# Kernel tuning notes

Hardware: AMD Instinct MI355X
Metric: run time of the kernel (lower is better)

## Reference

```python
import jax, jax.numpy as jnp
import numpy as np

N_EXPERTS = 64
LN_EPS = 1e-5


def _layer_norm(x, gamma, beta, eps=LN_EPS):
    mu = jnp.mean(x, axis=-1, keepdims=True)
    var = jnp.mean(jnp.square(x - mu), axis=-1, keepdims=True)
    return (x - mu) * jax.lax.rsqrt(var + eps) * gamma + beta


def setup_inputs() -> dict:
    key = jax.random.key(0)
    ks = jax.random.split(key, 4)
    B, T, D, Ff = 2, 1024, 512, 2048
    x = jax.random.normal(ks[0], (B, T, D), dtype=jnp.float32)
    hex_weights = jax.random.uniform(ks[1], (B, T, N_EXPERTS), dtype=jnp.float32)
    W_in = jax.random.normal(ks[2], (N_EXPERTS, Ff, D), dtype=jnp.float32) * (D ** -0.5)
    b_in = jnp.zeros((N_EXPERTS, Ff), dtype=jnp.float32)
    W_out = jax.random.normal(ks[3], (N_EXPERTS, D, Ff), dtype=jnp.float32) * (Ff ** -0.5)
    b_out = jnp.zeros((N_EXPERTS, D), dtype=jnp.float32)
    ln_gamma = jnp.ones((D,), dtype=jnp.float32)
    ln_beta = jnp.zeros((D,), dtype=jnp.float32)
    return {"x": x, "hex_weights": hex_weights, "W_in": W_in, "b_in": b_in,
            "W_out": W_out, "b_out": b_out, "ln_gamma": ln_gamma,
            "ln_beta": ln_beta, "top_k": 4}


def reference(x, hex_weights, W_in, b_in, W_out, b_out, ln_gamma, ln_beta, top_k):
    B, T, D = x.shape
    N = B * T
    x_n = _layer_norm(x, ln_gamma, ln_beta)

    # top-k routing; renormalize the selected weights (matches torch topk + sum-norm)
    top_w, top_idx = jax.lax.top_k(hex_weights, top_k)          # (B,T,k)
    top_w = top_w / (jnp.sum(top_w, axis=-1, keepdims=True) + 1e-8)

    x_flat = x_n.reshape(N, D)
    # Scatter the k normalized weights into a dense (N, 64) routing matrix.
    # Non-selected experts get weight 0, so a dense per-expert sweep computes
    # EXACTLY the same combined output as the per-token gather in the original.
    w_full = jnp.zeros((N, N_EXPERTS), dtype=x.dtype)
    w_full = w_full.at[jnp.arange(N)[:, None], top_idx.reshape(N, top_k)].set(
        top_w.reshape(N, top_k))

    def body(acc, e):
        W_in_e, b_in_e, W_out_e, b_out_e, we = e  # we: (N,)
        h = jax.nn.silu(x_flat @ W_in_e.T + b_in_e)            # (N, d_ff)
        acc = acc + we[:, None] * (h @ W_out_e.T + b_out_e)    # (N, D)
        return acc, None

    acc, _ = jax.lax.scan(body, jnp.zeros_like(x_flat),
                          (W_in, b_in, W_out, b_out, w_full.T))
    return acc.reshape(B, T, D)
```

## Files before the change

kernel.cpp:

```cpp
#include <hip/hip_runtime.h>

#define NTOK 2048
#define DD   512
#define FFD  2048
#define NE   64
#define KSEL 4
#define NPAIR (NTOK*KSEL)
#define BM 192
#define BN 128
#define BK 64
#define MAX_TILES 128
#define HROWS (NPAIR + 256)

typedef short s16x8 __attribute__((ext_vector_type(8)));
typedef float f32x4 __attribute__((ext_vector_type(4)));

typedef const __attribute__((address_space(1))) char* gptr_t;
typedef __attribute__((address_space(3))) char* lptr_t;

static __device__ __forceinline__ unsigned short f2bf(float f) {
    unsigned int u = __builtin_bit_cast(unsigned int, f);
    u += 0x7FFFu + ((u >> 16) & 1u);
    return (unsigned short)(u >> 16);
}

__global__ __launch_bounds__(256) void k_ln_route(
    const float* __restrict__ x, const float* __restrict__ hw,
    const float* __restrict__ gamma, const float* __restrict__ beta,
    unsigned short* __restrict__ xn_bf, int* __restrict__ counts,
    int* __restrict__ tok_e, float* __restrict__ tok_w)
{
    const int t = blockIdx.x;
    const int tid = threadIdx.x;
    const float* xr = x + (size_t)t * DD;
    float v0 = xr[tid];
    float v1 = xr[tid + 256];
    float s = v0 + v1, s2 = v0*v0 + v1*v1;
    #pragma unroll
    for (int off = 32; off > 0; off >>= 1) {
        s  += __shfl_down(s, off);
        s2 += __shfl_down(s2, off);
    }
    __shared__ float rsum[4], rsum2[4];
    __shared__ float smu, srs;
    const int wid = tid >> 6, lane = tid & 63;
    if (lane == 0) { rsum[wid] = s; rsum2[wid] = s2; }
    __syncthreads();
    if (tid == 0) {
        float a = 0.f, b = 0.f;
        for (int i = 0; i < 4; ++i) { a += rsum[i]; b += rsum2[i]; }
        float mu  = a * (1.f / DD);
        float var = b * (1.f / DD) - mu * mu;
        smu = mu; srs = rsqrtf(var + 1e-5f);
    }
    __syncthreads();
    const float mu = smu, rstd = srs;
    xn_bf[(size_t)t*DD + tid]       = f2bf((v0 - mu) * rstd * gamma[tid]       + beta[tid]);
    xn_bf[(size_t)t*DD + tid + 256] = f2bf((v1 - mu) * rstd * gamma[tid + 256] + beta[tid + 256]);

    if (tid < 64) {
        float v = hw[(size_t)t*NE + tid];
        int   sel[KSEL]; float sw[KSEL];
        #pragma unroll
        for (int j = 0; j < KSEL; ++j) {
            float m = v; int mi = tid;
            #pragma unroll
            for (int off = 32; off > 0; off >>= 1) {
                float ov = __shfl_xor(m, off);
                int   oi = __shfl_xor(mi, off);
                if (ov > m || (ov == m && oi < mi)) { m = ov; mi = oi; }
            }
            if (tid == mi) v = -1e30f;
            sel[j] = mi; sw[j] = m;
        }
        if (tid == 0) {
            float ssum = sw[0] + sw[1] + sw[2] + sw[3];
            float inv = 1.f / (ssum + 1e-8f);
            #pragma unroll
            for (int j = 0; j < KSEL; ++j) {
                tok_e[t*KSEL + j] = sel[j];
                tok_w[t*KSEL + j] = sw[j] * inv;
                atomicAdd(&counts[sel[j]], 1);
            }
        }
    }
}

__global__ void k_scan(const int* __restrict__ counts, int* __restrict__ offs,
                       int* __restrict__ cursor, int* __restrict__ tile_e,
                       int* __restrict__ tile_r, int* __restrict__ ntiles)
{
    __shared__ int sc[NE], stc[NE];
    const int tid = threadIdx.x;
    sc[tid] = counts[tid];
    __syncthreads();
    int off = 0;
    for (int i = 0; i < tid; ++i) off += sc[i];
    offs[tid] = off; cursor[tid] = off;
    if (tid == NE-1) offs[NE] = off + sc[NE-1];
    int tc = (sc[tid] + BM - 1) / BM;
    stc[tid] = tc;
    __syncthreads();
    int toff = 0;
    for (int i = 0; i < tid; ++i) toff += stc[i];
    for (int j = 0; j < tc; ++j) { tile_e[toff + j] = tid; tile_r[toff + j] = off + j*BM; }
    if (tid == NE-1) *ntiles = toff + tc;
}

__global__ __launch_bounds__(256) void k_scatter(
    const int* __restrict__ tok_e, const float* __restrict__ tok_w,
    int* __restrict__ cursor, int* __restrict__ pair_tok,
    float* __restrict__ pair_w, int* __restrict__ inv)
{
    int i = blockIdx.x * 256 + threadIdx.x;
    if (i >= NPAIR) return;
    int t = i >> 2;
    int e = tok_e[i];
    int slot = atomicAdd(&cursor[e], 1);
    pair_tok[slot] = t;
    pair_w[slot] = tok_w[i];
    inv[i] = slot;
}

template<int KD, bool IS_IN>
__global__ __launch_bounds__(256) void k_moe_gemm(
    const unsigned short* __restrict__ Abf,
    const float* __restrict__ W, const float* __restrict__ bias,
    const int* __restrict__ tile_e, const int* __restrict__ tile_r,
    const int* __restrict__ ntiles, const int* __restrict__ offs,
    const int* __restrict__ pr_tok, const float* __restrict__ pr_w,
    unsigned short* __restrict__ Hout, float* __restrict__ Pout)
{
    const int ti = blockIdx.x;
    if (ti >= *ntiles) return;
    const int e    = tile_e[ti];
    const int row0 = tile_r[ti];
    const int rend = offs[e + 1];
    const int n0   = blockIdx.y * BN;
    const int NOUT = IS_IN ? FFD : DD;
    const float* __restrict__ Wb = W + (size_t)e * NOUT * KD;

    __shared__ __align__(16) unsigned short As[BM * BK];
    __shared__ __align__(16) unsigned short Bs[BN * BK];

    const int tid  = threadIdx.x;
    const int lane = tid & 63, wave = tid >> 6;
    const int wm = wave >> 1, wn = wave & 1;

    const char* asrc[6];
    #pragma unroll
    for (int i = 0; i < 6; ++i) {
        int seg  = wave * 6 + i;
        int r    = seg * 8 + (lane >> 3);
        int grow = row0 + r;
        int cg   = (lane & 7) ^ (r & 7);
        size_t rowbase;
        if (IS_IN) {
            int tok = (grow < rend) ? pr_tok[grow] : 0;
            rowbase = (size_t)tok * (KD * 2);
        } else {
            rowbase = (size_t)grow * (KD * 2);
        }
        asrc[i] = (const char*)Abf + rowbase + (size_t)cg * 16;
    }

    f32x4 acc[6][4];
    #pragma unroll
    for (int m = 0; m < 6; ++m)
        #pragma unroll
        for (int n = 0; n < 4; ++n)
            acc[m][n] = (f32x4){0.f, 0.f, 0.f, 0.f};

    const float* wsrc0 = Wb + (size_t)(n0 + (tid >> 4)) * KD + (tid & 15) * 4;

    for (int k0 = 0; k0 < KD; k0 += BK) {
        float4 breg[8];
        #pragma unroll
        for (int i = 0; i < 8; ++i)
            breg[i] = *(const float4*)(wsrc0 + (size_t)i * 16 * KD + k0);

        __syncthreads();

        #pragma unroll
        for (int i = 0; i < 6; ++i) {
            __builtin_amdgcn_global_load_lds(
                (gptr_t)(asrc[i] + (size_t)k0 * 2),
                (lptr_t)((char*)As + (wave * 6 + i) * 1024),
                16, 0, 0);
        }

        {
            int nb = tid >> 4;
            int kb = (tid & 15) * 8;
            #pragma unroll
            for (int i = 0; i < 8; ++i) {
                int nn = nb + i * 16;
                unsigned int lo = (unsigned int)f2bf(breg[i].x) | ((unsigned int)f2bf(breg[i].y) << 16);
                unsigned int hi = (unsigned int)f2bf(breg[i].z) | ((unsigned int)f2bf(breg[i].w) << 16);
                int byte = nn * 128 + (kb ^ ((nn & 7) << 4));
                *(uint2*)((char*)Bs + byte) = make_uint2(lo, hi);
            }
        }

        __syncthreads();

        #pragma unroll
        for (int h = 0; h < 2; ++h) {
            s16x8 af[6], bf[4];
            const int koff = h * 64 + (lane >> 4) * 16;
            #pragma unroll
            for (int m = 0; m < 6; ++m) {
                int row = wm * 96 + m * 16 + (lane & 15);
                af[m] = *(const s16x8*)((const char*)As + row * 128 + (koff ^ ((row & 7) << 4)));
            }
            #pragma unroll
            for (int n = 0; n < 4; ++n) {
                int row = wn * 64 + n * 16 + (lane & 15);
                bf[n] = *(const s16x8*)((const char*)Bs + row * 128 + (koff ^ ((row & 7) << 4)));
            }
            #pragma unroll
            for (int m = 0; m < 6; ++m)
                #pragma unroll
                for (int n = 0; n < 4; ++n)
                    acc[m][n] = __builtin_amdgcn_mfma_f32_16x16x32_bf16(af[m], bf[n], acc[m][n], 0, 0, 0);
        }
    }

    #pragma unroll
    for (int m = 0; m < 6; ++m) {
        #pragma unroll
        for (int r = 0; r < 4; ++r) {
            int row = row0 + wm * 96 + m * 16 + (lane >> 4) * 4 + r;
            if (row < rend) {
                if (IS_IN) {
                    #pragma unroll
                    for (int n = 0; n < 4; ++n) {
                        int f = n0 + wn * 64 + n * 16 + (lane & 15);
                        float v = acc[m][n][r] + bias[e * FFD + f];
                        v = v / (1.f + __expf(-v));
                        Hout[(size_t)row * FFD + f] = f2bf(v);
                    }
                } else {
                    float pw = pr_w[row];
                    #pragma unroll
                    for (int n = 0; n < 4; ++n) {
                        int d = n0 + wn * 64 + n * 16 + (lane & 15);
                        Pout[(size_t)row * DD + d] = (acc[m][n][r] + bias[e * DD + d]) * pw;
                    }
                }
            }
        }
    }
}

__global__ __launch_bounds__(128) void k_combine(
    const float* __restrict__ pout, const int* __restrict__ inv,
    float* __restrict__ out)
{
    const int t = blockIdx.x;
    const int tid = threadIdx.x;
    const float4* p0 = (const float4*)(pout + (size_t)inv[t*4+0]*DD);
    const float4* p1 = (const float4*)(pout + (size_t)inv[t*4+1]*DD);
    const float4* p2 = (const float4*)(pout + (size_t)inv[t*4+2]*DD);
    const float4* p3 = (const float4*)(pout + (size_t)inv[t*4+3]*DD);
    float4 a = p0[tid], b = p1[tid], c = p2[tid], d = p3[tid];
    float4 r;
    r.x = a.x + b.x + c.x + d.x;
    r.y = a.y + b.y + c.y + d.y;
    r.z = a.z + b.z + c.z + d.z;
    r.w = a.w + b.w + c.w + d.w;
    ((float4*)(out + (size_t)t*DD))[tid] = r;
}

extern "C" void kernel_launch(void* const* d_in, const int* in_sizes, int n_in,
                              void* d_out, int out_size, void* d_ws, size_t ws_size,
                              hipStream_t stream)
{
    const float* x     = (const float*)d_in[0];
    const float* hw    = (const float*)d_in[1];
    const float* Win   = (const float*)d_in[2];
    const float* bin   = (const float*)d_in[3];
    const float* Wout  = (const float*)d_in[4];
    const float* bout  = (const float*)d_in[5];
    const float* gamma = (const float*)d_in[6];
    const float* beta  = (const float*)d_in[7];
    float* out = (float*)d_out;

    char* ws = (char*)d_ws;
    size_t o = 0;
    unsigned short* xn_bf = (unsigned short*)(ws + o); o += (size_t)NTOK * DD * 2;
    unsigned short* H     = (unsigned short*)(ws + o); o += (size_t)HROWS * FFD * 2;
    float* pout   = (float*)(ws + o); o += (size_t)NPAIR * DD * 4;
    int*   counts = (int*)(ws + o);   o += 256;
    int*   offs   = (int*)(ws + o);   o += 512;
    int*   cursor = (int*)(ws + o);   o += 256;
    int*   tok_e  = (int*)(ws + o);   o += (size_t)NPAIR * 4;
    float* tok_w  = (float*)(ws + o); o += (size_t)NPAIR * 4;
    int*   inv    = (int*)(ws + o);   o += (size_t)NPAIR * 4;
    int*   pr_tok = (int*)(ws + o);   o += (size_t)NPAIR * 4;
    float* pr_w   = (float*)(ws + o); o += (size_t)NPAIR * 4;
    int*   tile_e = (int*)(ws + o);   o += 512;
    int*   tile_r = (int*)(ws + o);   o += 512;
    int*   ntiles = (int*)(ws + o);   o += 256;
    (void)ws_size; (void)in_sizes; (void)n_in; (void)out_size;

    hipMemsetAsync(counts, 0, 256, stream);
    k_ln_route<<<dim3(NTOK), dim3(256), 0, stream>>>(x, hw, gamma, beta, xn_bf, counts, tok_e, tok_w);
    k_scan<<<dim3(1), dim3(64), 0, stream>>>(counts, offs, cursor, tile_e, tile_r, ntiles);
    k_scatter<<<dim3(NPAIR/256), dim3(256), 0, stream>>>(tok_e, tok_w, cursor, pr_tok, pr_w, inv);

    dim3 gA(MAX_TILES, FFD / BN);
    k_moe_gemm<DD, true><<<gA, dim3(256), 0, stream>>>(
        xn_bf, Win, bin, tile_e, tile_r, ntiles, offs, pr_tok, pr_w, H, nullptr);
    dim3 gB(MAX_TILES, DD / BN);
    k_moe_gemm<FFD, false><<<gB, dim3(256), 0, stream>>>(
        H, Wout, bout, tile_e, tile_r, ntiles, offs, pr_tok, pr_w, nullptr, pout);

    k_combine<<<dim3(NTOK), dim3(128), 0, stream>>>(pout, inv, out);
}
```

Baseline: 254.0 us.

## Double-buffer MoE GEMM LDS tiles and narrow down-projection N tile

Adds double-buffered LDS for the A and B tiles so the loads for the next K step are issued before the MFMA work on the current step, with one barrier per iteration instead of two. The down-projection GEMM now uses a 64-wide N tile with each wave owning 48 rows, which doubles its grid along N so more blocks fill the GPU. Launch bounds now request two blocks per SIMD. In exchange, LDS use doubles and the prefetched weight registers increase register pressure, which could limit occupancy.

```diff
diff --git a/kernel.cpp b/kernel.cpp
--- a/kernel.cpp
+++ b/kernel.cpp
@@ -7,7 +7,6 @@
 #define KSEL 4
 #define NPAIR (NTOK*KSEL)
 #define BM 192
-#define BN 128
 #define BK 64
 #define MAX_TILES 128
 #define HROWS (NPAIR + 256)
@@ -22,6 +21,12 @@
     unsigned int u = __builtin_bit_cast(unsigned int, f);
     u += 0x7FFFu + ((u >> 16) & 1u);
     return (unsigned short)(u >> 16);
+}
+
+static __device__ __forceinline__ void packwrite(char* base, int nn, int kb, float4 v) {
+    unsigned int lo = (unsigned int)f2bf(v.x) | ((unsigned int)f2bf(v.y) << 16);
+    unsigned int hi = (unsigned int)f2bf(v.z) | ((unsigned int)f2bf(v.w) << 16);
+    *(uint2*)(base + nn * 128 + (kb ^ ((nn & 7) << 4))) = make_uint2(lo, hi);
 }
 
 __global__ __launch_bounds__(256) void k_ln_route(
@@ -122,8 +127,8 @@
     inv[i] = slot;
 }
 
-template<int KD, bool IS_IN>
-__global__ __launch_bounds__(256) void k_moe_gemm(
+template<int KD, bool IS_IN, int BNX>
+__global__ __launch_bounds__(256, 2) void k_moe_gemm(
     const unsigned short* __restrict__ Abf,
     const float* __restrict__ W, const float* __restrict__ bias,
     const int* __restrict__ tile_e, const int* __restrict__ tile_r,
@@ -131,21 +136,25 @@
     const int* __restrict__ pr_tok, const float* __restrict__ pr_w,
     unsigned short* __restrict__ Hout, float* __restrict__ Pout)
 {
+    constexpr int NK = KD / BK;
+    constexpr int NB = BNX / 16;
+    constexpr int MT = IS_IN ? 6 : 3;
     const int ti = blockIdx.x;
     if (ti >= *ntiles) return;
     const int e    = tile_e[ti];
     const int row0 = tile_r[ti];
     const int rend = offs[e + 1];
-    const int n0   = blockIdx.y * BN;
+    const int n0   = blockIdx.y * BNX;
     const int NOUT = IS_IN ? FFD : DD;
     const float* __restrict__ Wb = W + (size_t)e * NOUT * KD;
 
-    __shared__ __align__(16) unsigned short As[BM * BK];
-    __shared__ __align__(16) unsigned short Bs[BN * BK];
+    __shared__ __align__(16) unsigned short As[2 * BM * BK];
+    __shared__ __align__(16) unsigned short Bs[2 * BNX * BK];
 
     const int tid  = threadIdx.x;
     const int lane = tid & 63, wave = tid >> 6;
-    const int wm = wave >> 1, wn = wave & 1;
+    const int wmbase = IS_IN ? (wave >> 1) * 96 : wave * 48;
+    const int wnbase = IS_IN ? (wave & 1) * 64 : 0;
 
     const char* asrc[6];
     #pragma unroll
@@ -164,78 +173,92 @@
         asrc[i] = (const char*)Abf + rowbase + (size_t)cg * 16;
     }
 
-    f32x4 acc[6][4];
+    const float* wsrc0 = Wb + (size_t)(n0 + (tid >> 4)) * KD + (tid & 15) * 4;
+    const int nb = tid >> 4;
+    const int kb = (tid & 15) * 8;
+
+    f32x4 acc[MT][4];
     #pragma unroll
-    for (int m = 0; m < 6; ++m)
+    for (int m = 0; m < MT; ++m)
         #pragma unroll
         for (int n = 0; n < 4; ++n)
             acc[m][n] = (f32x4){0.f, 0.f, 0.f, 0.f};
 
-    const float* wsrc0 = Wb + (size_t)(n0 + (tid >> 4)) * KD + (tid & 15) * 4;
-
-    for (int k0 = 0; k0 < KD; k0 += BK) {
-        float4 breg[8];
-        #pragma unroll
-        for (int i = 0; i < 8; ++i)
-            breg[i] = *(const float4*)(wsrc0 + (size_t)i * 16 * KD + k0);
-
-        __syncthreads();
-
-        #pragma unroll
-        for (int i = 0; i < 6; ++i) {
-            __builtin_amdgcn_global_load_lds(
-                (gptr_t)(asrc[i] + (size_t)k0 * 2),
-                (lptr_t)((char*)As + (wave * 6 + i) * 1024),
-                16, 0, 0);
-        }
-
-        {
-            int nb = tid >> 4;
-            int kb = (tid & 15) * 8;
-            #pragma unroll
-            for (int i = 0; i < 8; ++i) {
-                int nn = nb + i * 16;
-                unsigned int lo = (unsigned int)f2bf(breg[i].x) | ((unsigned int)f2bf(breg[i].y) << 16);
-                unsigned int hi = (unsigned int)f2bf(breg[i].z) | ((unsigned int)f2bf(breg[i].w) << 16);
-                int byte = nn * 128 + (kb ^ ((nn & 7) << 4));
-                *(uint2*)((char*)Bs + byte) = make_uint2(lo, hi);
-            }
-        }
-
-        __syncthreads();
-
+    {
+        #pragma unroll
+        for (int i = 0; i < 6; ++i)
+            __builtin_amdgcn_global_load_lds((gptr_t)asrc[i],
+                (lptr_t)((char*)As + (wave * 6 + i) * 1024), 16, 0, 0);
+        float4 breg[NB];
+        #pragma unroll
+        for (int i = 0; i < NB; ++i)
+            breg[i] = *(const float4*)(wsrc0 + (size_t)i * 16 * KD);
+        #pragma unroll
+        for (int i = 0; i < NB; ++i)
+            packwrite((char*)Bs, nb + i * 16, kb, breg[i]);
+    }
+    __syncthreads();
+
+    int buf = 0;
+    for (int kt = 0; kt < NK; ++kt) {
+        const int k0n = (kt + 1) * BK;
+        float4 bregN[NB];
+        if (kt + 1 < NK) {
+            #pragma unroll
+            for (int i = 0; i < 6; ++i)
+                __builtin_amdgcn_global_load_lds((gptr_t)(asrc[i] + (size_t)k0n * 2),
+                    (lptr_t)((char*)As + (buf ^ 1) * (BM * BK * 2) + (wave * 6 + i) * 1024),
+                    16, 0, 0);
+            #pragma unroll
+            for (int i = 0; i < NB; ++i)
+                bregN[i] = *(const float4*)(wsrc0 + (size_t)i * 16 * KD + k0n);
+        }
+        __builtin_amdgcn_sched_barrier(0);
+
+        const char* Ab = (const char*)As + buf * (BM * BK * 2);
+        const char* Bb = (const char*)Bs + buf * (BNX * BK * 2);
         #pragma unroll
         for (int h = 0; h < 2; ++h) {
-            s16x8 af[6], bf[4];
+            s16x8 af[MT], bfr[4];
             const int koff = h * 64 + (lane >> 4) * 16;
             #pragma unroll
-            for (int m = 0; m < 6; ++m) {
-                int row = wm * 96 + m * 16 + (lane & 15);
-                af[m] = *(const s16x8*)((const char*)As + row * 128 + (koff ^ ((row & 7) << 4)));
+            for (int m = 0; m < MT; ++m) {
+                int row = wmbase + m * 16 + (lane & 15);
+                af[m] = *(const s16x8*)(Ab + row * 128 + (koff ^ ((row & 7) << 4)));
             }
             #pragma unroll
             for (int n = 0; n < 4; ++n) {
-                int row = wn * 64 + n * 16 + (lane & 15);
-                bf[n] = *(const s16x8*)((const char*)Bs + row * 128 + (koff ^ ((row & 7) << 4)));
-            }
-            #pragma unroll
-            for (int m = 0; m < 6; ++m)
+                int row = wnbase + n * 16 + (lane & 15);
+                bfr[n] = *(const s16x8*)(Bb + row * 128 + (koff ^ ((row & 7) << 4)));
+            }
+            #pragma unroll
+            for (int m = 0; m < MT; ++m)
                 #pragma unroll
                 for (int n = 0; n < 4; ++n)
-                    acc[m][n] = __builtin_amdgcn_mfma_f32_16x16x32_bf16(af[m], bf[n], acc[m][n], 0, 0, 0);
-        }
+                    acc[m][n] = __builtin_amdgcn_mfma_f32_16x16x32_bf16(af[m], bfr[n], acc[m][n], 0, 0, 0);
+        }
+        __builtin_amdgcn_sched_barrier(0);
+
+        if (kt + 1 < NK) {
+            char* Bw = (char*)Bs + (buf ^ 1) * (BNX * BK * 2);
+            #pragma unroll
+            for (int i = 0; i < NB; ++i)
+                packwrite(Bw, nb + i * 16, kb, bregN[i]);
+        }
+        __syncthreads();
+        buf ^= 1;
     }
 
     #pragma unroll
-    for (int m = 0; m < 6; ++m) {
+    for (int m = 0; m < MT; ++m) {
         #pragma unroll
         for (int r = 0; r < 4; ++r) {
-            int row = row0 + wm * 96 + m * 16 + (lane >> 4) * 4 + r;
+            int row = row0 + wmbase + m * 16 + (lane >> 4) * 4 + r;
             if (row < rend) {
                 if (IS_IN) {
                     #pragma unroll
                     for (int n = 0; n < 4; ++n) {
-                        int f = n0 + wn * 64 + n * 16 + (lane & 15);
+                        int f = n0 + wnbase + n * 16 + (lane & 15);
                         float v = acc[m][n][r] + bias[e * FFD + f];
                         v = v / (1.f + __expf(-v));
                         Hout[(size_t)row * FFD + f] = f2bf(v);
@@ -244,7 +267,7 @@
                     float pw = pr_w[row];
                     #pragma unroll
                     for (int n = 0; n < 4; ++n) {
-                        int d = n0 + wn * 64 + n * 16 + (lane & 15);
+                        int d = n0 + wnbase + n * 16 + (lane & 15);
                         Pout[(size_t)row * DD + d] = (acc[m][n][r] + bias[e * DD + d]) * pw;
                     }
                 }
@@ -309,11 +332,11 @@
     k_scan<<<dim3(1), dim3(64), 0, stream>>>(counts, offs, cursor, tile_e, tile_r, ntiles);
     k_scatter<<<dim3(NPAIR/256), dim3(256), 0, stream>>>(tok_e, tok_w, cursor, pr_tok, pr_w, inv);
 
-    dim3 gA(MAX_TILES, FFD / BN);
-    k_moe_gemm<DD, true><<<gA, dim3(256), 0, stream>>>(
+    dim3 gA(MAX_TILES, FFD / 128);
+    k_moe_gemm<DD, true, 128><<<gA, dim3(256), 0, stream>>>(
         xn_bf, Win, bin, tile_e, tile_r, ntiles, offs, pr_tok, pr_w, H, nullptr);
-    dim3 gB(MAX_TILES, DD / BN);
-    k_moe_gemm<FFD, false><<<gB, dim3(256), 0, stream>>>(
+    dim3 gB(MAX_TILES, DD / 64);
+    k_moe_gemm<FFD, false, 64><<<gB, dim3(256), 0, stream>>>(
         H, Wout, bout, tile_e, tile_r, ntiles, offs, pr_tok, pr_w, nullptr, pout);
 
     k_combine<<<dim3(NTOK), dim3(128), 0, stream>>>(pout, inv, out);
```

New measurement: 242.8 us. 4.4% less time.

## Restructure MoE GEMMs to stream fp32 weights once per expert into registers

Applied to the files above, without the earlier changes.

Replaces the tile-list MoE GEMM with per-expert blocks that each own a slice of output columns and loop over all token rows. Weights are read directly from global memory into registers and converted to bf16 on the fly, with no LDS staging and no barriers. The activations come straight from global memory per MFMA fragment. The second GEMM splits K into two halves for more parallelism, writing two partial outputs that the combine kernel sums. This aims to read each weight only once and make the weight-bandwidth-bound GEMMs stream better. The cost is uncoalesced, uncached-in-LDS activation loads and extra partial-output traffic.

```diff
diff --git a/kernel.cpp b/kernel.cpp
--- a/kernel.cpp
+++ b/kernel.cpp
@@ -6,22 +6,23 @@
 #define NE   64
 #define KSEL 4
 #define NPAIR (NTOK*KSEL)
-#define BM 192
-#define BN 128
-#define BK 64
-#define MAX_TILES 128
-#define HROWS (NPAIR + 256)
 
 typedef short s16x8 __attribute__((ext_vector_type(8)));
 typedef float f32x4 __attribute__((ext_vector_type(4)));
-
-typedef const __attribute__((address_space(1))) char* gptr_t;
-typedef __attribute__((address_space(3))) char* lptr_t;
 
 static __device__ __forceinline__ unsigned short f2bf(float f) {
     unsigned int u = __builtin_bit_cast(unsigned int, f);
     u += 0x7FFFu + ((u >> 16) & 1u);
     return (unsigned short)(u >> 16);
+}
+
+static __device__ __forceinline__ s16x8 cvt8(float4 a, float4 b) {
+    s16x8 r;
+    r[0] = (short)f2bf(a.x); r[1] = (short)f2bf(a.y);
+    r[2] = (short)f2bf(a.z); r[3] = (short)f2bf(a.w);
+    r[4] = (short)f2bf(b.x); r[5] = (short)f2bf(b.y);
+    r[6] = (short)f2bf(b.z); r[7] = (short)f2bf(b.w);
+    return r;
 }
 
 __global__ __launch_bounds__(256) void k_ln_route(
@@ -87,10 +88,9 @@
 }
 
 __global__ void k_scan(const int* __restrict__ counts, int* __restrict__ offs,
-                       int* __restrict__ cursor, int* __restrict__ tile_e,
-                       int* __restrict__ tile_r, int* __restrict__ ntiles)
-{
-    __shared__ int sc[NE], stc[NE];
+                       int* __restrict__ cursor)
+{
+    __shared__ int sc[NE];
     const int tid = threadIdx.x;
     sc[tid] = counts[tid];
     __syncthreads();
@@ -98,13 +98,6 @@
     for (int i = 0; i < tid; ++i) off += sc[i];
     offs[tid] = off; cursor[tid] = off;
     if (tid == NE-1) offs[NE] = off + sc[NE-1];
-    int tc = (sc[tid] + BM - 1) / BM;
-    stc[tid] = tc;
-    __syncthreads();
-    int toff = 0;
-    for (int i = 0; i < tid; ++i) toff += stc[i];
-    for (int j = 0; j < tc; ++j) { tile_e[toff + j] = tid; tile_r[toff + j] = off + j*BM; }
-    if (tid == NE-1) *ntiles = toff + tc;
 }
 
 __global__ __launch_bounds__(256) void k_scatter(
@@ -122,130 +115,169 @@
     inv[i] = slot;
 }
 
-template<int KD, bool IS_IN>
-__global__ __launch_bounds__(256) void k_moe_gemm(
-    const unsigned short* __restrict__ Abf,
-    const float* __restrict__ W, const float* __restrict__ bias,
-    const int* __restrict__ tile_e, const int* __restrict__ tile_r,
-    const int* __restrict__ ntiles, const int* __restrict__ offs,
-    const int* __restrict__ pr_tok, const float* __restrict__ pr_w,
-    unsigned short* __restrict__ Hout, float* __restrict__ Pout)
-{
-    const int ti = blockIdx.x;
-    if (ti >= *ntiles) return;
-    const int e    = tile_e[ti];
-    const int row0 = tile_r[ti];
-    const int rend = offs[e + 1];
-    const int n0   = blockIdx.y * BN;
-    const int NOUT = IS_IN ? FFD : DD;
-    const float* __restrict__ Wb = W + (size_t)e * NOUT * KD;
-
-    __shared__ __align__(16) unsigned short As[BM * BK];
-    __shared__ __align__(16) unsigned short Bs[BN * BK];
-
-    const int tid  = threadIdx.x;
-    const int lane = tid & 63, wave = tid >> 6;
-    const int wm = wave >> 1, wn = wave & 1;
-
-    const char* asrc[6];
-    #pragma unroll
-    for (int i = 0; i < 6; ++i) {
-        int seg  = wave * 6 + i;
-        int r    = seg * 8 + (lane >> 3);
-        int grow = row0 + r;
-        int cg   = (lane & 7) ^ (r & 7);
-        size_t rowbase;
-        if (IS_IN) {
-            int tok = (grow < rend) ? pr_tok[grow] : 0;
-            rowbase = (size_t)tok * (KD * 2);
-        } else {
-            rowbase = (size_t)grow * (KD * 2);
-        }
-        asrc[i] = (const char*)Abf + rowbase + (size_t)cg * 16;
-    }
-
-    f32x4 acc[6][4];
-    #pragma unroll
-    for (int m = 0; m < 6; ++m)
-        #pragma unroll
-        for (int n = 0; n < 4; ++n)
-            acc[m][n] = (f32x4){0.f, 0.f, 0.f, 0.f};
-
-    const float* wsrc0 = Wb + (size_t)(n0 + (tid >> 4)) * KD + (tid & 15) * 4;
-
-    for (int k0 = 0; k0 < KD; k0 += BK) {
-        float4 breg[8];
-        #pragma unroll
-        for (int i = 0; i < 8; ++i)
-            breg[i] = *(const float4*)(wsrc0 + (size_t)i * 16 * KD + k0);
-
-        __syncthreads();
-
-        #pragma unroll
-        for (int i = 0; i < 6; ++i) {
-            __builtin_amdgcn_global_load_lds(
-                (gptr_t)(asrc[i] + (size_t)k0 * 2),
-                (lptr_t)((char*)As + (wave * 6 + i) * 1024),
-                16, 0, 0);
-        }
-
-        {
-            int nb = tid >> 4;
-            int kb = (tid & 15) * 8;
+__global__ __launch_bounds__(256, 2) void k_gemm_in(
+    const unsigned short* __restrict__ xn, const float* __restrict__ Win,
+    const float* __restrict__ bin, const int* __restrict__ offs,
+    const int* __restrict__ pr_tok, unsigned short* __restrict__ H)
+{
+    const int b  = blockIdx.x;
+    const int e  = (b & 7) * 8 + ((b >> 3) & 7);
+    const int ng = b >> 6;
+    const int tid = threadIdx.x;
+    const int lane = tid & 63, w = tid >> 6;
+    const int n0 = ng * 128 + w * 32;
+    const int row0 = offs[e], rend = offs[e + 1];
+    const int cnt = rend - row0;
+    const int lr = lane & 15, lk = lane >> 4;
+
+    const float* __restrict__ wrow0 = Win + (size_t)e * FFD * DD + (size_t)(n0 + lr) * DD + lk * 8;
+    const float* __restrict__ wrow1 = wrow0 + (size_t)16 * DD;
+
+    for (int m0 = 0; m0 < cnt; m0 += 192) {
+        const unsigned short* aptr[12];
+        #pragma unroll
+        for (int mf = 0; mf < 12; ++mf) {
+            int row = row0 + m0 + mf * 16 + lr;
+            int rowc = row < rend ? row : row0;
+            int tok = pr_tok[rowc];
+            aptr[mf] = xn + (size_t)tok * DD + lk * 8;
+        }
+
+        f32x4 acc[12][2];
+        #pragma unroll
+        for (int mf = 0; mf < 12; ++mf) {
+            acc[mf][0] = (f32x4){0.f,0.f,0.f,0.f};
+            acc[mf][1] = (f32x4){0.f,0.f,0.f,0.f};
+        }
+
+        float4 c00 = *(const float4*)(wrow0);
+        float4 c01 = *(const float4*)(wrow0 + 4);
+        float4 c10 = *(const float4*)(wrow1);
+        float4 c11 = *(const float4*)(wrow1 + 4);
+
+        #pragma unroll 2
+        for (int kt = 0; kt < 16; ++kt) {
+            float4 n00, n01, n10, n11;
+            if (kt + 1 < 16) {
+                int ko = (kt + 1) * 32;
+                n00 = *(const float4*)(wrow0 + ko);
+                n01 = *(const float4*)(wrow0 + ko + 4);
+                n10 = *(const float4*)(wrow1 + ko);
+                n11 = *(const float4*)(wrow1 + ko + 4);
+            }
+            s16x8 bf0 = cvt8(c00, c01);
+            s16x8 bf1 = cvt8(c10, c11);
             #pragma unroll
-            for (int i = 0; i < 8; ++i) {
-                int nn = nb + i * 16;
-                unsigned int lo = (unsigned int)f2bf(breg[i].x) | ((unsigned int)f2bf(breg[i].y) << 16);
-                unsigned int hi = (unsigned int)f2bf(breg[i].z) | ((unsigned int)f2bf(breg[i].w) << 16);
-                int byte = nn * 128 + (kb ^ ((nn & 7) << 4));
-                *(uint2*)((char*)Bs + byte) = make_uint2(lo, hi);
-            }
-        }
-
-        __syncthreads();
-
-        #pragma unroll
-        for (int h = 0; h < 2; ++h) {
-            s16x8 af[6], bf[4];
-            const int koff = h * 64 + (lane >> 4) * 16;
+            for (int mf = 0; mf < 12; ++mf) {
+                if (m0 + mf * 16 < cnt) {
+                    s16x8 af = *(const s16x8*)(aptr[mf] + kt * 32);
+                    acc[mf][0] = __builtin_amdgcn_mfma_f32_16x16x32_bf16(af, bf0, acc[mf][0], 0, 0, 0);
+                    acc[mf][1] = __builtin_amdgcn_mfma_f32_16x16x32_bf16(af, bf1, acc[mf][1], 0, 0, 0);
+                }
+            }
+            c00 = n00; c01 = n01; c10 = n10; c11 = n11;
+        }
+
+        #pragma unroll
+        for (int mf = 0; mf < 12; ++mf) {
+            if (m0 + mf * 16 < cnt) {
+                #pragma unroll
+                for (int r = 0; r < 4; ++r) {
+                    int row = row0 + m0 + mf * 16 + lk * 4 + r;
+                    if (row < rend) {
+                        #pragma unroll
+                        for (int nf = 0; nf < 2; ++nf) {
+                            int f = n0 + nf * 16 + lr;
+                            float v = acc[mf][nf][r] + bin[e * FFD + f];
+                            v = v / (1.f + __expf(-v));
+                            H[(size_t)row * FFD + f] = f2bf(v);
+                        }
+                    }
+                }
+            }
+        }
+    }
+}
+
+__global__ __launch_bounds__(128, 2) void k_gemm_out(
+    const unsigned short* __restrict__ H, const float* __restrict__ Wout,
+    const float* __restrict__ bout, const int* __restrict__ offs,
+    const float* __restrict__ pr_w, float* __restrict__ pout)
+{
+    const int b  = blockIdx.x;
+    const int e  = (b & 7) * 8 + ((b >> 3) & 7);
+    const int j  = b >> 6;
+    const int ng = j & 7, z = j >> 3;
+    const int tid = threadIdx.x;
+    const int lane = tid & 63, w = tid >> 6;
+    const int n0 = ng * 64 + w * 32;
+    const int row0 = offs[e], rend = offs[e + 1];
+    const int cnt = rend - row0;
+    const int lr = lane & 15, lk = lane >> 4;
+    const int kbase = z * 1024;
+
+    const float* __restrict__ wrow0 = Wout + (size_t)e * DD * FFD + (size_t)(n0 + lr) * FFD + kbase + lk * 8;
+    const float* __restrict__ wrow1 = wrow0 + (size_t)16 * FFD;
+
+    for (int m0 = 0; m0 < cnt; m0 += 192) {
+        const unsigned short* aptr[12];
+        #pragma unroll
+        for (int mf = 0; mf < 12; ++mf) {
+            int row = row0 + m0 + mf * 16 + lr;
+            int rowc = row < rend ? row : row0;
+            aptr[mf] = H + (size_t)rowc * FFD + kbase + lk * 8;
+        }
+
+        f32x4 acc[12][2];
+        #pragma unroll
+        for (int mf = 0; mf < 12; ++mf) {
+            acc[mf][0] = (f32x4){0.f,0.f,0.f,0.f};
+            acc[mf][1] = (f32x4){0.f,0.f,0.f,0.f};
+        }
+
+        float4 c00 = *(const float4*)(wrow0);
+        float4 c01 = *(const float4*)(wrow0 + 4);
+        float4 c10 = *(const float4*)(wrow1);
+        float4 c11 = *(const float4*)(wrow1 + 4);
+
+        #pragma unroll 2
+        for (int kt = 0; kt < 32; ++kt) {
+            float4 n00, n01, n10, n11;
+            if (kt + 1 < 32) {
+                int ko = (kt + 1) * 32;
+                n00 = *(const float4*)(wrow0 + ko);
+                n01 = *(const float4*)(wrow0 + ko + 4);
+                n10 = *(const float4*)(wrow1 + ko);
+                n11 = *(const float4*)(wrow1 + ko + 4);
+            }
+            s16x8 bf0 = cvt8(c00, c01);
+            s16x8 bf1 = cvt8(c10, c11);
             #pragma unroll
-            for (int m = 0; m < 6; ++m) {
-                int row = wm * 96 + m * 16 + (lane & 15);
-                af[m] = *(const s16x8*)((const char*)As + row * 128 + (koff ^ ((row & 7) << 4)));
-            }
-            #pragma unroll
-            for (int n = 0; n < 4; ++n) {
-                int row = wn * 64 + n * 16 + (lane & 15);
-                bf[n] = *(const s16x8*)((const char*)Bs + row * 128 + (koff ^ ((row & 7) << 4)));
-            }
-            #pragma unroll
-            for (int m = 0; m < 6; ++m)
+            for (int mf = 0; mf < 12; ++mf) {
+                if (m0 + mf * 16 < cnt) {
+                    s16x8 af = *(const s16x8*)(aptr[mf] + kt * 32);
+                    acc[mf][0] = __builtin_amdgcn_mfma_f32_16x16x32_bf16(af, bf0, acc[mf][0], 0, 0, 0);
+                    acc[mf][1] = __builtin_amdgcn_mfma_f32_16x16x32_bf16(af, bf1, acc[mf][1], 0, 0, 0);
+                }
+            }
+            c00 = n00; c01 = n01; c10 = n10; c11 = n11;
+        }
+
+        #pragma unroll
+        for (int mf = 0; mf < 12; ++mf) {
+            if (m0 + mf * 16 < cnt) {
                 #pragma unroll
-                for (int n = 0; n < 4; ++n)
-                    acc[m][n] = __builtin_amdgcn_mfma_f32_16x16x32_bf16(af[m], bf[n], acc[m][n], 0, 0, 0);
-        }
-    }
-
-    #pragma unroll
-    for (int m = 0; m < 6; ++m) {
-        #pragma unroll
-        for (int r = 0; r < 4; ++r) {
-            int row = row0 + wm * 96 + m * 16 + (lane >> 4) * 4 + r;
-            if (row < rend) {
-                if (IS_IN) {
-                    #pragma unroll
-                    for (int n = 0; n < 4; ++n) {
-                        int f = n0 + wn * 64 + n * 16 + (lane & 15);
-                        float v = acc[m][n][r] + bias[e * FFD + f];
-                        v = v / (1.f + __expf(-v));
-                        Hout[(size_t)row * FFD + f] = f2bf(v);
-                    }
-                } else {
-                    float pw = pr_w[row];
-                    #pragma unroll
-                    for (int n = 0; n < 4; ++n) {
-                        int d = n0 + wn * 64 + n * 16 + (lane & 15);
-                        Pout[(size_t)row * DD + d] = (acc[m][n][r] + bias[e * DD + d]) * pw;
+                for (int r = 0; r < 4; ++r) {
+                    int row = row0 + m0 + mf * 16 + lk * 4 + r;
+                    if (row < rend) {
+                        float pw = pr_w[row];
+                        #pragma unroll
+                        for (int nf = 0; nf < 2; ++nf) {
+                            int d = n0 + nf * 16 + lr;
+                            float v = acc[mf][nf][r];
+                            if (z == 0) v += bout[e * DD + d];
+                            pout[((size_t)z * NPAIR + row) * DD + d] = v * pw;
+                        }
                     }
                 }
             }
@@ -259,16 +291,14 @@
 {
     const int t = blockIdx.x;
     const int tid = threadIdx.x;
-    const float4* p0 = (const float4*)(pout + (size_t)inv[t*4+0]*DD);
-    const float4* p1 = (const float4*)(pout + (size_t)inv[t*4+1]*DD);
-    const float4* p2 = (const float4*)(pout + (size_t)inv[t*4+2]*DD);
-    const float4* p3 = (const float4*)(pout + (size_t)inv[t*4+3]*DD);
-    float4 a = p0[tid], b = p1[tid], c = p2[tid], d = p3[tid];
-    float4 r;
-    r.x = a.x + b.x + c.x + d.x;
-    r.y = a.y + b.y + c.y + d.y;
-    r.z = a.z + b.z + c.z + d.z;
-    r.w = a.w + b.w + c.w + d.w;
+    float4 r = {0.f, 0.f, 0.f, 0.f};
+    #pragma unroll
+    for (int j = 0; j < 4; ++j) {
+        size_t slot = (size_t)inv[t*4 + j];
+        float4 a = ((const float4*)(pout + slot * DD))[tid];
+        float4 b = ((const float4*)(pout + ((size_t)NPAIR + slot) * DD))[tid];
+        r.x += a.x + b.x; r.y += a.y + b.y; r.z += a.z + b.z; r.w += a.w + b.w;
+    }
     ((float4*)(out + (size_t)t*DD))[tid] = r;
 }
 
@@ -289,8 +319,8 @@
     char* ws = (char*)d_ws;
     size_t o = 0;
     unsigned short* xn_bf = (unsigned short*)(ws + o); o += (size_t)NTOK * DD * 2;
-    unsigned short* H     = (unsigned short*)(ws + o); o += (size_t)HROWS * FFD * 2;
-    float* pout   = (float*)(ws + o); o += (size_t)NPAIR * DD * 4;
+    unsigned short* H     = (unsigned short*)(ws + o); o += (size_t)NPAIR * FFD * 2;
+    float* pout   = (float*)(ws + o); o += (size_t)2 * NPAIR * DD * 4;
     int*   counts = (int*)(ws + o);   o += 256;
     int*   offs   = (int*)(ws + o);   o += 512;
     int*   cursor = (int*)(ws + o);   o += 256;
@@ -299,22 +329,15 @@
     int*   inv    = (int*)(ws + o);   o += (size_t)NPAIR * 4;
     int*   pr_tok = (int*)(ws + o);   o += (size_t)NPAIR * 4;
     float* pr_w   = (float*)(ws + o); o += (size_t)NPAIR * 4;
-    int*   tile_e = (int*)(ws + o);   o += 512;
-    int*   tile_r = (int*)(ws + o);   o += 512;
-    int*   ntiles = (int*)(ws + o);   o += 256;
     (void)ws_size; (void)in_sizes; (void)n_in; (void)out_size;
 
     hipMemsetAsync(counts, 0, 256, stream);
     k_ln_route<<<dim3(NTOK), dim3(256), 0, stream>>>(x, hw, gamma, beta, xn_bf, counts, tok_e, tok_w);
-    k_scan<<<dim3(1), dim3(64), 0, stream>>>(counts, offs, cursor, tile_e, tile_r, ntiles);
+    k_scan<<<dim3(1), dim3(64), 0, stream>>>(counts, offs, cursor);
     k_scatter<<<dim3(NPAIR/256), dim3(256), 0, stream>>>(tok_e, tok_w, cursor, pr_tok, pr_w, inv);
 
-    dim3 gA(MAX_TILES, FFD / BN);
-    k_moe_gemm<DD, true><<<gA, dim3(256), 0, stream>>>(
-        xn_bf, Win, bin, tile_e, tile_r, ntiles, offs, pr_tok, pr_w, H, nullptr);
-    dim3 gB(MAX_TILES, DD / BN);
-    k_moe_gemm<FFD, false><<<gB, dim3(256), 0, stream>>>(
-        H, Wout, bout, tile_e, tile_r, ntiles, offs, pr_tok, pr_w, nullptr, pout);
+    k_gemm_in<<<dim3(1024), dim3(256), 0, stream>>>(xn_bf, Win, bin, offs, pr_tok, H);
+    k_gemm_out<<<dim3(1024), dim3(128), 0, stream>>>(H, Wout, bout, offs, pr_w, pout);
 
     k_combine<<<dim3(NTOK), dim3(128), 0, stream>>>(pout, inv, out);
 }
```

Result: slower. 380.1 us (+49.6%).

## Software-pipeline MoE GEMM with triple-buffered A and double-buffered converted weights

Applied to the files above, without the earlier changes.

Restructures the grouped MoE GEMM into a software pipeline. The K step drops to 32, with a triple-buffered LDS ring for the routed activation tile and a double-buffered bf16 weight tile. Weight loads are issued two steps ahead, and hand-placed waitcnt and sched barriers overlap global loads with MFMA work. The N tile shrinks from 128 to 64 and each wave owns 48 rows, giving more blocks and an occupancy hint of 3 per SIMD. Together these aim to hide the latency of the fp32 weight load and conversion. The risk is fragile manual vmcnt accounting and less operand reuse per block.

```diff
diff --git a/kernel.cpp b/kernel.cpp
--- a/kernel.cpp
+++ b/kernel.cpp
@@ -7,9 +7,7 @@
 #define KSEL 4
 #define NPAIR (NTOK*KSEL)
 #define BM 192
-#define BN 128
-#define BK 64
-#define MAX_TILES 128
+#define NT 128
 #define HROWS (NPAIR + 256)
 
 typedef short s16x8 __attribute__((ext_vector_type(8)));
@@ -22,6 +20,15 @@
     unsigned int u = __builtin_bit_cast(unsigned int, f);
     u += 0x7FFFu + ((u >> 16) & 1u);
     return (unsigned short)(u >> 16);
+}
+
+static __device__ __forceinline__ s16x8 cvt8(float4 a, float4 b) {
+    s16x8 r;
+    r[0] = (short)f2bf(a.x); r[1] = (short)f2bf(a.y);
+    r[2] = (short)f2bf(a.z); r[3] = (short)f2bf(a.w);
+    r[4] = (short)f2bf(b.x); r[5] = (short)f2bf(b.y);
+    r[6] = (short)f2bf(b.z); r[7] = (short)f2bf(b.w);
+    return r;
 }
 
 __global__ __launch_bounds__(256) void k_ln_route(
@@ -123,7 +130,7 @@
 }
 
 template<int KD, bool IS_IN>
-__global__ __launch_bounds__(256) void k_moe_gemm(
+__global__ __launch_bounds__(256, 3) void k_moe_gemm(
     const unsigned short* __restrict__ Abf,
     const float* __restrict__ W, const float* __restrict__ bias,
     const int* __restrict__ tile_e, const int* __restrict__ tile_r,
@@ -131,32 +138,33 @@
     const int* __restrict__ pr_tok, const float* __restrict__ pr_w,
     unsigned short* __restrict__ Hout, float* __restrict__ Pout)
 {
-    const int ti = blockIdx.x;
+    constexpr int NK = KD / 32;
+    const int ti = blockIdx.x & (NT - 1);
+    const int yg = blockIdx.x >> 7;
     if (ti >= *ntiles) return;
     const int e    = tile_e[ti];
     const int row0 = tile_r[ti];
     const int rend = offs[e + 1];
-    const int n0   = blockIdx.y * BN;
+    const int n0   = yg * 64;
     const int NOUT = IS_IN ? FFD : DD;
-    const float* __restrict__ Wb = W + (size_t)e * NOUT * KD;
-
-    __shared__ __align__(16) unsigned short As[BM * BK];
-    __shared__ __align__(16) unsigned short Bs[BN * BK];
+
+    __shared__ __align__(16) unsigned short As[3 * BM * 32];
+    __shared__ __align__(16) unsigned short Bs[2 * 64 * 32];
 
     const int tid  = threadIdx.x;
     const int lane = tid & 63, wave = tid >> 6;
-    const int wm = wave >> 1, wn = wave & 1;
-
-    const char* asrc[6];
-    #pragma unroll
-    for (int i = 0; i < 6; ++i) {
-        int seg  = wave * 6 + i;
-        int r    = seg * 8 + (lane >> 3);
+    const int lr = lane & 15, lk = lane >> 4;
+
+    const char* asrc[3];
+    #pragma unroll
+    for (int i = 0; i < 3; ++i) {
+        int seg  = wave * 3 + i;
+        int r    = seg * 16 + (lane >> 2);
+        int cg   = (lane & 3) ^ ((lane >> 2) & 3);
         int grow = row0 + r;
-        int cg   = (lane & 7) ^ (r & 7);
         size_t rowbase;
         if (IS_IN) {
-            int tok = (grow < rend) ? pr_tok[grow] : 0;
+            int tok = (grow < rend) ? pr_tok[grow] : pr_tok[row0];
             rowbase = (size_t)tok * (KD * 2);
         } else {
             rowbase = (size_t)grow * (KD * 2);
@@ -164,78 +172,102 @@
         asrc[i] = (const char*)Abf + rowbase + (size_t)cg * 16;
     }
 
-    f32x4 acc[6][4];
-    #pragma unroll
-    for (int m = 0; m < 6; ++m)
+    const float* wptr = W + (size_t)e * NOUT * KD + (size_t)(n0 + (tid >> 2)) * KD + (tid & 3) * 8;
+    char* bdst0 = (char*)Bs + (tid >> 2) * 64 + (((tid & 3) ^ ((tid >> 2) & 3)) << 4);
+
+    f32x4 acc[3][4];
+    #pragma unroll
+    for (int m = 0; m < 3; ++m)
         #pragma unroll
         for (int n = 0; n < 4; ++n)
             acc[m][n] = (f32x4){0.f, 0.f, 0.f, 0.f};
 
-    const float* wsrc0 = Wb + (size_t)(n0 + (tid >> 4)) * KD + (tid & 15) * 4;
-
-    for (int k0 = 0; k0 < KD; k0 += BK) {
-        float4 breg[8];
-        #pragma unroll
-        for (int i = 0; i < 8; ++i)
-            breg[i] = *(const float4*)(wsrc0 + (size_t)i * 16 * KD + k0);
-
-        __syncthreads();
-
-        #pragma unroll
-        for (int i = 0; i < 6; ++i) {
-            __builtin_amdgcn_global_load_lds(
-                (gptr_t)(asrc[i] + (size_t)k0 * 2),
-                (lptr_t)((char*)As + (wave * 6 + i) * 1024),
-                16, 0, 0);
-        }
-
-        {
-            int nb = tid >> 4;
-            int kb = (tid & 15) * 8;
-            #pragma unroll
-            for (int i = 0; i < 8; ++i) {
-                int nn = nb + i * 16;
-                unsigned int lo = (unsigned int)f2bf(breg[i].x) | ((unsigned int)f2bf(breg[i].y) << 16);
-                unsigned int hi = (unsigned int)f2bf(breg[i].z) | ((unsigned int)f2bf(breg[i].w) << 16);
-                int byte = nn * 128 + (kb ^ ((nn & 7) << 4));
-                *(uint2*)((char*)Bs + byte) = make_uint2(lo, hi);
-            }
-        }
-
-        __syncthreads();
-
-        #pragma unroll
-        for (int h = 0; h < 2; ++h) {
-            s16x8 af[6], bf[4];
-            const int koff = h * 64 + (lane >> 4) * 16;
-            #pragma unroll
-            for (int m = 0; m < 6; ++m) {
-                int row = wm * 96 + m * 16 + (lane & 15);
-                af[m] = *(const s16x8*)((const char*)As + row * 128 + (koff ^ ((row & 7) << 4)));
-            }
-            #pragma unroll
-            for (int n = 0; n < 4; ++n) {
-                int row = wn * 64 + n * 16 + (lane & 15);
-                bf[n] = *(const s16x8*)((const char*)Bs + row * 128 + (koff ^ ((row & 7) << 4)));
-            }
-            #pragma unroll
-            for (int m = 0; m < 6; ++m)
-                #pragma unroll
-                for (int n = 0; n < 4; ++n)
-                    acc[m][n] = __builtin_amdgcn_mfma_f32_16x16x32_bf16(af[m], bf[n], acc[m][n], 0, 0, 0);
-        }
-    }
-
-    #pragma unroll
-    for (int m = 0; m < 6; ++m) {
+    float4 waA0, waA1, waB0, waB1;
+
+    waA0 = *(const float4*)(wptr);
+    waA1 = *(const float4*)(wptr + 4);
+    asm volatile("s_waitcnt vmcnt(0)" ::: "memory");
+    __builtin_amdgcn_sched_barrier(0);
+    *(s16x8*)bdst0 = cvt8(waA0, waA1);
+    #pragma unroll
+    for (int i = 0; i < 3; ++i)
+        __builtin_amdgcn_global_load_lds((gptr_t)asrc[i],
+            (lptr_t)((char*)As + (wave * 3 + i) * 1024), 16, 0, 0);
+    __builtin_amdgcn_sched_barrier(0);
+    waB0 = *(const float4*)(wptr + 32);
+    waB1 = *(const float4*)(wptr + 36);
+    __builtin_amdgcn_sched_barrier(0);
+    #pragma unroll
+    for (int i = 0; i < 3; ++i)
+        __builtin_amdgcn_global_load_lds((gptr_t)(asrc[i] + 64),
+            (lptr_t)((char*)As + 12288 + (wave * 3 + i) * 1024), 16, 0, 0);
+
+    int ab0 = 0, ab1 = 1, ab2 = 2;
+
+#define GEMM_STEP(KT, WUSE0, WUSE1, WISS0, WISS1)                                        \
+    {                                                                                    \
+        if ((KT) == NK - 1) asm volatile("s_waitcnt vmcnt(0) lgkmcnt(0)" ::: "memory");  \
+        else                asm volatile("s_waitcnt vmcnt(5) lgkmcnt(0)" ::: "memory");  \
+        __builtin_amdgcn_s_barrier();                                                    \
+        __builtin_amdgcn_sched_barrier(0);                                               \
+        if ((KT) + 2 < NK) {                                                             \
+            WISS0 = *(const float4*)(wptr + ((KT) + 2) * 32);                            \
+            WISS1 = *(const float4*)(wptr + ((KT) + 2) * 32 + 4);                        \
+        }                                                                                \
+        __builtin_amdgcn_sched_barrier(0);                                               \
+        if ((KT) + 2 < NK) {                                                             \
+            _Pragma("unroll")                                                            \
+            for (int i = 0; i < 3; ++i)                                                  \
+                __builtin_amdgcn_global_load_lds(                                        \
+                    (gptr_t)(asrc[i] + (size_t)((KT) + 2) * 64),                         \
+                    (lptr_t)((char*)As + ab2 * 12288 + (wave * 3 + i) * 1024),           \
+                    16, 0, 0);                                                           \
+        }                                                                                \
+        __builtin_amdgcn_sched_barrier(0);                                               \
+        {                                                                                \
+            const char* Ab = (const char*)As + ab0 * 12288;                              \
+            const char* Bb = (const char*)Bs + ((KT) & 1) * 4096;                        \
+            const int sw = ((lk ^ (lr & 3)) << 4);                                       \
+            s16x8 af[3], bfr[4];                                                         \
+            _Pragma("unroll")                                                            \
+            for (int m = 0; m < 3; ++m)                                                  \
+                af[m] = *(const s16x8*)(Ab + (wave * 48 + m * 16 + lr) * 64 + sw);       \
+            _Pragma("unroll")                                                            \
+            for (int n = 0; n < 4; ++n)                                                  \
+                bfr[n] = *(const s16x8*)(Bb + (n * 16 + lr) * 64 + sw);                  \
+            _Pragma("unroll")                                                            \
+            for (int m = 0; m < 3; ++m)                                                  \
+                _Pragma("unroll")                                                        \
+                for (int n = 0; n < 4; ++n)                                              \
+                    acc[m][n] = __builtin_amdgcn_mfma_f32_16x16x32_bf16(                 \
+                        af[m], bfr[n], acc[m][n], 0, 0, 0);                              \
+        }                                                                                \
+        __builtin_amdgcn_sched_barrier(0);                                               \
+        if ((KT) + 1 < NK) {                                                             \
+            if ((KT) + 2 < NK) asm volatile("s_waitcnt vmcnt(8)" ::: "memory");          \
+            else               asm volatile("s_waitcnt vmcnt(3)" ::: "memory");          \
+            __builtin_amdgcn_sched_barrier(0);                                           \
+            *(s16x8*)(bdst0 + (((KT) + 1) & 1) * 4096) = cvt8(WUSE0, WUSE1);             \
+        }                                                                                \
+        int tmp_ = ab0; ab0 = ab1; ab1 = ab2; ab2 = tmp_;                                \
+    }
+
+    for (int kt = 0; kt < NK; kt += 2) {
+        GEMM_STEP(kt,     waB0, waB1, waA0, waA1);
+        GEMM_STEP(kt + 1, waA0, waA1, waB0, waB1);
+    }
+#undef GEMM_STEP
+
+    #pragma unroll
+    for (int m = 0; m < 3; ++m) {
         #pragma unroll
         for (int r = 0; r < 4; ++r) {
-            int row = row0 + wm * 96 + m * 16 + (lane >> 4) * 4 + r;
+            int row = row0 + wave * 48 + m * 16 + lk * 4 + r;
             if (row < rend) {
                 if (IS_IN) {
                     #pragma unroll
                     for (int n = 0; n < 4; ++n) {
-                        int f = n0 + wn * 64 + n * 16 + (lane & 15);
+                        int f = n0 + n * 16 + lr;
                         float v = acc[m][n][r] + bias[e * FFD + f];
                         v = v / (1.f + __expf(-v));
                         Hout[(size_t)row * FFD + f] = f2bf(v);
@@ -244,7 +276,7 @@
                     float pw = pr_w[row];
                     #pragma unroll
                     for (int n = 0; n < 4; ++n) {
-                        int d = n0 + wn * 64 + n * 16 + (lane & 15);
+                        int d = n0 + n * 16 + lr;
                         Pout[(size_t)row * DD + d] = (acc[m][n][r] + bias[e * DD + d]) * pw;
                     }
                 }
@@ -309,11 +341,9 @@
     k_scan<<<dim3(1), dim3(64), 0, stream>>>(counts, offs, cursor, tile_e, tile_r, ntiles);
     k_scatter<<<dim3(NPAIR/256), dim3(256), 0, stream>>>(tok_e, tok_w, cursor, pr_tok, pr_w, inv);
 
-    dim3 gA(MAX_TILES, FFD / BN);
-    k_moe_gemm<DD, true><<<gA, dim3(256), 0, stream>>>(
+    k_moe_gemm<DD, true><<<dim3(NT * (FFD/64)), dim3(256), 0, stream>>>(
         xn_bf, Win, bin, tile_e, tile_r, ntiles, offs, pr_tok, pr_w, H, nullptr);
-    dim3 gB(MAX_TILES, DD / BN);
-    k_moe_gemm<FFD, false><<<gB, dim3(256), 0, stream>>>(
+    k_moe_gemm<FFD, false><<<dim3(NT * (DD/64)), dim3(256), 0, stream>>>(
         H, Wout, bout, tile_e, tile_r, ntiles, offs, pr_tok, pr_w, nullptr, pout);
 
     k_combine<<<dim3(NTOK), dim3(128), 0, stream>>>(pout, inv, out);
```

Measured after the change: 287.7 us. +13.2%, slower.
